# Performance work log

Hardware: AMD Instinct MI355X
Metric: run time of the kernel (lower is better)

Reference implementation:

```python
import jax, jax.numpy as jnp
import numpy as np

B, N, K = 4, 4096, 16
DP, DM = 64, 128
EPS = 1e-8


def setup_inputs() -> dict:
    key = jax.random.key(0)
    ks = jax.random.split(key, 32)
    g = lambda i, shape, fan: jax.random.normal(ks[i], shape, jnp.float32) / np.sqrt(fan)
    inp = {
        'xyz': jax.random.normal(ks[0], (B, N, 3), jnp.float32),
        'features': jax.random.normal(ks[1], (B, N, DP), jnp.float32),
        # fc1: d_points -> d_model
        'fc1_w': g(2, (DP, DM), DP), 'fc1_b': jnp.zeros((DM,), jnp.float32),
        # fc2: d_model -> d_points
        'fc2_w': g(3, (DM, DP), DM), 'fc2_b': jnp.zeros((DP,), jnp.float32),
        # fc_delta: Linear(3,DM) -> ReLU -> Linear(DM,DM)
        'd1_w': g(4, (3, DM), 3), 'd1_b': jnp.zeros((DM,), jnp.float32),
        'd2_w': g(5, (DM, DM), DM), 'd2_b': jnp.zeros((DM,), jnp.float32),
        # fc_gamma: Linear(DM,DM) -> ReLU -> Linear(DM,DM)
        'g1_w': g(6, (DM, DM), DM), 'g1_b': jnp.zeros((DM,), jnp.float32),
        'g2_w': g(7, (DM, DM), DM), 'g2_b': jnp.zeros((DM,), jnp.float32),
        # q/k/v projections, no bias
        'wq_w': g(8, (DM, DM), DM), 'wk_w': g(9, (DM, DM), DM), 'wv_w': g(10, (DM, DM), DM),
        # fc_sim: Linear(DM+1, DM)
        'sim_w': g(11, (DM + 1, DM), DM + 1), 'sim_b': jnp.zeros((DM,), jnp.float32),
    }
    return inp


def _gather(t, idx):
    # t: [B, N, C], idx: [B, N, K] -> [B, N, K, C]
    bidx = jnp.arange(t.shape[0])[:, None, None]
    return t[bidx, idx]


def reference(xyz, features, fc1_w, fc1_b, fc2_w, fc2_b, d1_w, d1_b, d2_w, d2_b,
              g1_w, g1_b, g2_w, g2_b, wq_w, wk_w, wv_w, sim_w, sim_b):
    # pairwise squared distances [B, N, N]
    sq = jnp.sum(xyz * xyz, axis=-1)
    dists = sq[:, :, None] + sq[:, None, :] - 2.0 * jnp.einsum('bnc,bmc->bnm', xyz, xyz)
    knn_idx = jnp.argsort(dists, axis=-1)[:, :, :K]            # [B, N, K]

    knn_xyz = _gather(xyz, knn_idx)                            # [B, N, K, 3]
    x = features @ fc1_w + fc1_b                               # [B, N, DM]
    q = x @ wq_w                                               # [B, N, DM]
    k = _gather(x @ wk_w, knn_idx)                             # [B, N, K, DM]
    v = _gather(x @ wv_w, knn_idx)                             # [B, N, K, DM]

    rel_pos = xyz[:, :, None, :] - knn_xyz                     # [B, N, K, 3]
    pos_enc = jax.nn.relu(rel_pos @ d1_w + d1_b) @ d2_w + d2_b # [B, N, K, DM]

    qe = q[:, :, None, :]                                      # [B, N, 1, DM]
    # torch cosine_similarity: dot / (max(||q||,eps) * max(||k||,eps))
    qn = jnp.maximum(jnp.linalg.norm(q, axis=-1), EPS)[:, :, None]
    kn = jnp.maximum(jnp.linalg.norm(k, axis=-1), EPS)
    sim = jnp.sum(qe * k, axis=-1) / (qn * kn)                 # [B, N, K]

    rel_qk = jnp.concatenate([sim[..., None], qe - k], axis=-1)  # [B, N, K, DM+1]
    rel_qk = rel_qk @ sim_w + sim_b                            # [B, N, K, DM]

    attn = jax.nn.relu((rel_qk + pos_enc) @ g1_w + g1_b) @ g2_w + g2_b
    attn = jax.nn.softmax(attn / np.sqrt(DM).astype(np.float32), axis=-2)  # over K

    res = jnp.einsum('bnkf,bnkf->bnf', attn, v + pos_enc)      # [B, N, DM]
    res = res @ fc2_w + fc2_b + features                       # [B, N, DP]
    return res, attn
```

## Files before the change

### kernel.cpp

```cpp
#include <hip/hip_runtime.h>
#include <hip/hip_bf16.h>

#define BB 4
#define NN 4096
#define KK 16
#define DP 64
#define DM 128
#define DMP 132
#define EPSF 1e-8f
#define OUT0N ((size_t)BB * NN * DP)

typedef unsigned short u16t;
typedef __attribute__((ext_vector_type(8))) short s8v;
typedef __attribute__((ext_vector_type(4))) float f4v;

__device__ int g_flag;

__device__ __forceinline__ float u2f(u16t u) {
    unsigned int x = ((unsigned int)u) << 16;
    return __uint_as_float(x);
}
__device__ __forceinline__ u16t f2u(float v) {
    __hip_bfloat16 h = __float2bfloat16(v);
    return *(u16t*)&h;
}

template<int DT> struct IO;
template<> struct IO<0> {
    static __device__ __forceinline__ float ld(const void* p, size_t i) { return ((const float*)p)[i]; }
    static __device__ __forceinline__ void ld4(const void* p, size_t i, float o[4]) {
        float4 v = *(const float4*)((const float*)p + i);
        o[0] = v.x; o[1] = v.y; o[2] = v.z; o[3] = v.w;
    }
    static __device__ __forceinline__ void st(void* p, size_t i, float v) { ((float*)p)[i] = v; }
};
template<> struct IO<1> {
    static __device__ __forceinline__ float ld(const void* p, size_t i) { return u2f(((const u16t*)p)[i]); }
    static __device__ __forceinline__ void ld4(const void* p, size_t i, float o[4]) {
        ushort4 v = *(const ushort4*)((const u16t*)p + i);
        o[0] = u2f(v.x); o[1] = u2f(v.y); o[2] = u2f(v.z); o[3] = u2f(v.w);
    }
    static __device__ __forceinline__ void st(void* p, size_t i, float v) { ((u16t*)p)[i] = f2u(v); }
};

__global__ __launch_bounds__(64) void detect_kernel(const void* feat) {
    const int tid = threadIdx.x;
    float x = u2f(((const u16t*)feat)[2 * tid]);
    float a = fabsf(x);
    bool sane = (x == 0.0f) || (a > 1e-4f && a < 50.0f);
    unsigned long long m = __ballot(sane);
    if (tid == 0) g_flag = (__popcll(m) >= 32) ? 1 : 0;
}

struct QkvSmem { float sf[DP]; float sx[DM]; };

template<int DT>
__device__ __forceinline__ void qkv_body(QkvSmem& s,
    const void* feat, const void* fc1_w, const void* fc1_b,
    const void* wq, const void* wk, const void* wv,
    float* __restrict__ qbuf, float* __restrict__ kbuf, float* __restrict__ vbuf)
{
    const int bn = blockIdx.x;
    const int tid = threadIdx.x;
    if (tid < DP) s.sf[tid] = IO<DT>::ld(feat, (size_t)bn * DP + tid);
    __syncthreads();
    float x = IO<DT>::ld(fc1_b, tid);
#pragma unroll 4
    for (int i = 0; i < DP; i++) x = fmaf(s.sf[i], IO<DT>::ld(fc1_w, i * DM + tid), x);
    s.sx[tid] = x;
    __syncthreads();
    float q = 0.f, k = 0.f, v = 0.f;
    for (int i0 = 0; i0 < DM; i0 += 4) {
        float4 xv = *(const float4*)&s.sx[i0];
        const float xs[4] = { xv.x, xv.y, xv.z, xv.w };
#pragma unroll
        for (int j = 0; j < 4; j++) {
            q = fmaf(xs[j], IO<DT>::ld(wq, (i0 + j) * DM + tid), q);
            k = fmaf(xs[j], IO<DT>::ld(wk, (i0 + j) * DM + tid), k);
            v = fmaf(xs[j], IO<DT>::ld(wv, (i0 + j) * DM + tid), v);
        }
    }
    qbuf[(size_t)bn * DM + tid] = q;
    kbuf[(size_t)bn * DM + tid] = k;
    vbuf[(size_t)bn * DM + tid] = v;
}

__global__ __launch_bounds__(128) void qkv_kernel(
    const void* feat, const void* fc1_w, const void* fc1_b,
    const void* wq, const void* wk, const void* wv,
    float* qbuf, float* kbuf, float* vbuf)
{
    __shared__ __align__(16) QkvSmem s;
    if (g_flag) qkv_body<1>(s, feat, fc1_w, fc1_b, wq, wk, wv, qbuf, kbuf, vbuf);
    else        qkv_body<0>(s, feat, fc1_w, fc1_b, wq, wk, wv, qbuf, kbuf, vbuf);
}

template<int DT>
__device__ __forceinline__ void knn_body(float4* __restrict__ sc,
    const void* xyz, int* dst, int dstride, void* dout, int in_out)
{
    if (in_out) {
        if (DT) { dst = (int*)((u16t*)dout + OUT0N); dstride = (KK * DM) / 2; }
        else    { dst = (int*)((float*)dout + OUT0N); dstride = KK * DM; }
    }
    const int b = blockIdx.x >> 9;
    const int tid = threadIdx.x;
    for (int j = tid; j < NN; j += 512) {
        float x = IO<DT>::ld(xyz, ((size_t)b * NN + j) * 3 + 0);
        float y = IO<DT>::ld(xyz, ((size_t)b * NN + j) * 3 + 1);
        float z = IO<DT>::ld(xyz, ((size_t)b * NN + j) * 3 + 2);
        float sq = __fadd_rn(__fadd_rn(__fmul_rn(x, x), __fmul_rn(y, y)), __fmul_rn(z, z));
        sc[j] = make_float4(x, y, z, sq);
    }
    __syncthreads();
    const int lane = tid & 63;
    const int wave = tid >> 6;
    const int r = ((blockIdx.x & 511) << 3) + wave;
    const float4 qc = sc[r];

    float d[KK];
    int id[KK];
#pragma unroll
    for (int t = 0; t < KK; t++) { d[t] = 3.4e38f; id[t] = 0x7fffffff; }

    for (int j = lane; j < NN; j += 64) {
        const float4 c = sc[j];
        const float dot = __fadd_rn(__fadd_rn(__fmul_rn(qc.x, c.x), __fmul_rn(qc.y, c.y)),
                                    __fmul_rn(qc.z, c.z));
        const float dist = __fsub_rn(__fadd_rn(qc.w, c.w), __fmul_rn(2.0f, dot));
        if (dist < d[KK - 1]) {
            float cd = dist; int ci = j;
#pragma unroll
            for (int t = 0; t < KK; t++) {
                const bool sw = (cd < d[t]);
                const float od = d[t]; const int oi = id[t];
                d[t]  = sw ? cd : d[t];
                id[t] = sw ? ci : id[t];
                cd = sw ? od : cd;
                ci = sw ? oi : ci;
            }
        }
    }

    const size_t base = (size_t)(b * NN + r) * (size_t)dstride;
#pragma unroll
    for (int t = 0; t < KK; t++) {
        float bd = d[0]; int bi = id[0];
#pragma unroll
        for (int off = 32; off >= 1; off >>= 1) {
            const float od = __shfl_xor(bd, off, 64);
            const int   oi = __shfl_xor(bi, off, 64);
            if (od < bd || (od == bd && oi < bi)) { bd = od; bi = oi; }
        }
        const bool win = (d[0] == bd) && (id[0] == bi);
        if (win) {
#pragma unroll
            for (int u = 0; u < KK - 1; u++) { d[u] = d[u + 1]; id[u] = id[u + 1]; }
            d[KK - 1] = 3.4e38f; id[KK - 1] = 0x7fffffff;
        }
        if (lane == t) dst[base + t] = bi;
    }
}

__global__ __launch_bounds__(512) void knn_kernel(
    const void* xyz, int* dst, int dstride, void* dout, int in_out)
{
    __shared__ __align__(16) float4 sc[NN];
    if (g_flag) knn_body<1>(sc, xyz, dst, dstride, dout, in_out);
    else        knn_body<0>(sc, xyz, dst, dstride, dout, in_out);
}

template<int DT>
__device__ __forceinline__ void gemm_tile(const float* __restrict__ IN,
                                          const void* __restrict__ W, int woff,
                                          int kg, int f0, float acc[4][4])
{
#pragma unroll
    for (int a = 0; a < 4; a++)
#pragma unroll
        for (int c = 0; c < 4; c++) acc[a][c] = 0.f;
    for (int i0 = 0; i0 < DM; i0 += 4) {
        float w[4][4];
#pragma unroll
        for (int j = 0; j < 4; j++) IO<DT>::ld4(W, (size_t)woff + (i0 + j) * DM + f0, w[j]);
#pragma unroll
        for (int kk = 0; kk < 4; kk++) {
            float4 x4 = *(const float4*)(IN + (kg * 4 + kk) * DMP + i0);
            const float xs[4] = { x4.x, x4.y, x4.z, x4.w };
#pragma unroll
            for (int ff = 0; ff < 4; ff++)
#pragma unroll
                for (int j = 0; j < 4; j++)
                    acc[kk][ff] = fmaf(xs[j], w[j][ff], acc[kk][ff]);
        }
    }
}

template<int DT>
__device__ __forceinline__ void wprep_body(const void* sim_w, const void* d2_w,
                                           const void* g1_w, const void* g2_w,
                                           u16t* __restrict__ wprep)
{
    const int m  = blockIdx.x >> 3;
    const int t  = blockIdx.x & 7;
    const int ks = threadIdx.x >> 6;
    const int lane = threadIdx.x & 63;
    const void* src = (m == 0) ? sim_w : (m == 1) ? d2_w : (m == 2) ? g1_w : g2_w;
    const int srcoff = (m == 0) ? DM : 0;
    u16t* hi = wprep + (size_t)m * 32768;
    u16t* lo = hi + 16384;
    const int c  = t * 16 + (lane & 15);
    const int k0 = ks * 32 + ((lane >> 4) << 3);
    s8v vh, vl;
#pragma unroll
    for (int j = 0; j < 8; j++) {
        const float x = IO<DT>::ld(src, (size_t)srcoff + (size_t)(k0 + j) * DM + c);
        const u16t h = f2u(x);
        vh[j] = (short)h;
        vl[j] = (short)f2u(x - u2f(h));
    }
    const size_t off = ((size_t)(t * 4 + ks) * 64 + lane) * 8;
    *(s8v*)(hi + off) = vh;
    *(s8v*)(lo + off) = vl;
}

__global__ __launch_bounds__(256) void wprep_kernel(
    const void* sim_w, const void* d2_w, const void* g1_w, const void* g2_w,
    u16t* wprep)
{
    if (g_flag) wprep_body<1>(sim_w, d2_w, g1_w, g2_w, wprep);
    else        wprep_body<0>(sim_w, d2_w, g1_w, g2_w, wprep);
}

template<int DT, int EPI>
__device__ __forceinline__ void mfma_gemm16(const float* __restrict__ IN,
                                            float* __restrict__ OUT,
                                            const u16t* __restrict__ wmat,
                                            const void* bias, const void* w0,
                                            const float* __restrict__ ssim)
{
    const int tid  = threadIdx.x;
    const int lane = tid & 63;
    const int wid  = tid >> 6;
    const u16t* whi = wmat;
    const u16t* wlo = wmat + 16384;
    f4v acc[4] = { {0.f,0.f,0.f,0.f}, {0.f,0.f,0.f,0.f}, {0.f,0.f,0.f,0.f}, {0.f,0.f,0.f,0.f} };
    const float* ain = IN + (size_t)(lane & 15) * DMP + ((lane >> 4) << 3);
#pragma unroll
    for (int ks = 0; ks < 4; ks++) {
        const float4 x0 = *(const float4*)(ain + ks * 32);
        const float4 x1 = *(const float4*)(ain + ks * 32 + 4);
        const float xs[8] = { x0.x, x0.y, x0.z, x0.w, x1.x, x1.y, x1.z, x1.w };
        s8v ahi, alo;
#pragma unroll
        for (int j = 0; j < 8; j++) {
            const u16t h = f2u(xs[j]);
            ahi[j] = (short)h;
            alo[j] = (short)f2u(xs[j] - u2f(h));
        }
#pragma unroll
        for (int t = 0; t < 4; t++) {
            const size_t off = ((size_t)((wid * 4 + t) * 4 + ks) * 64 + lane) * 8;
            const s8v bhi = *(const s8v*)(whi + off);
            const s8v blo = *(const s8v*)(wlo + off);
            acc[t] = __builtin_amdgcn_mfma_f32_16x16x32_bf16(ahi, bhi, acc[t], 0, 0, 0);
            acc[t] = __builtin_amdgcn_mfma_f32_16x16x32_bf16(ahi, blo, acc[t], 0, 0, 0);
            acc[t] = __builtin_amdgcn_mfma_f32_16x16x32_bf16(alo, bhi, acc[t], 0, 0, 0);
        }
    }
    const int r0 = (lane >> 4) * 4;
#pragma unroll
    for (int t = 0; t < 4; t++) {
        const int col = (wid * 4 + t) * 16 + (lane & 15);
        const float bv = IO<DT>::ld(bias, col);
        float w0v = 0.f;
        if constexpr (EPI == 2) w0v = IO<DT>::ld(w0, col);
#pragma unroll
        for (int r = 0; r < 4; r++) {
            float v = acc[t][r] + bv;
            if constexpr (EPI == 2) v = fmaf(ssim[r0 + r], w0v, v);
            if constexpr (EPI == 1) v = fmaxf(v, 0.f);
            OUT[(size_t)(r0 + r) * DMP + col] = v;
        }
    }
}

struct AttnSmemM {
    float KP[KK * DMP];
    float T0[KK * DMP];
    float T1[KK * DMP];
    float s_q[DM], sres[DM];
    float srp[KK][3];
    float ssim[KK], skn[KK], sdot[KK];
    float sqn;
    int sidx[KK];
};

template<int DT>
__device__ __forceinline__ void attn_mfma_body(AttnSmemM& s,
    const void* xyz, const void* feat,
    const void* fc2_w, const void* fc2_b,
    const void* d1_w, const void* d1_b, const void* d2_b,
    const void* g1_b, const void* g2_b,
    const void* sim_w, const void* sim_b,
    const float* __restrict__ qbuf, const float* __restrict__ kbuf,
    const float* __restrict__ vbuf,
    const int* __restrict__ knn, const u16t* __restrict__ wprep, void* dout)
{
    void* out0 = dout;
    void* out1 = DT ? (void*)((u16t*)dout + OUT0N) : (void*)((float*)dout + OUT0N);
    const int bn = blockIdx.x;
    const int b = bn >> 12;
    const int tid = threadIdx.x;
    const int f = tid;

    if (tid < KK) {
        int sv = knn[(size_t)bn * KK + tid];
        sv = (sv < 0) ? 0 : (sv > NN - 1 ? NN - 1 : sv);
        s.sidx[tid] = sv;
    }
    __syncthreads();

    s.s_q[f] = qbuf[(size_t)bn * DM + f];
#pragma unroll
    for (int k = 0; k < KK; k++) {
        const int row = (b << 12) + s.sidx[k];
        s.KP[k * DMP + f] = kbuf[(size_t)row * DM + f];
    }
    if (tid < KK) {
        const int row = (b << 12) + s.sidx[tid];
#pragma unroll
        for (int c = 0; c < 3; c++)
            s.srp[tid][c] = IO<DT>::ld(xyz, (size_t)bn * 3 + c) - IO<DT>::ld(xyz, (size_t)row * 3 + c);
    }
    __syncthreads();

    {
        const int j = tid >> 3, g = tid & 7;
        float sk = 0.f, sd = 0.f, qq = 0.f;
#pragma unroll
        for (int i = 0; i < 16; i++) {
            const int ff = g * 16 + i;
            const float kv = s.KP[j * DMP + ff];
            const float qv = s.s_q[ff];
            sk = fmaf(kv, kv, sk);
            sd = fmaf(qv, kv, sd);
            qq = fmaf(qv, qv, qq);
        }
#pragma unroll
        for (int off = 1; off <= 4; off <<= 1) {
            sk += __shfl_xor(sk, off, 64);
            sd += __shfl_xor(sd, off, 64);
            qq += __shfl_xor(qq, off, 64);
        }
        if (g == 0) { s.skn[j] = fmaxf(sqrtf(sk), EPSF); s.sdot[j] = sd; }
        if (tid == 0) s.sqn = fmaxf(sqrtf(qq), EPSF);
    }
    __syncthreads();

    if (tid < KK) s.ssim[tid] = s.sdot[tid] / (s.sqn * s.skn[tid]);
#pragma unroll
    for (int k = 0; k < KK; k++) s.T0[k * DMP + f] = s.s_q[f] - s.KP[k * DMP + f];
    __syncthreads();

    mfma_gemm16<DT, 2>(s.T0, s.T1, wprep + 0 * 32768, sim_b, sim_w, s.ssim);
    __syncthreads();

    {
        const float w0 = IO<DT>::ld(d1_w, 0 * DM + f), w1 = IO<DT>::ld(d1_w, 1 * DM + f),
                    w2 = IO<DT>::ld(d1_w, 2 * DM + f);
        const float hb = IO<DT>::ld(d1_b, f);
#pragma unroll
        for (int k = 0; k < KK; k++) {
            const float h = fmaf(s.srp[k][2], w2, fmaf(s.srp[k][1], w1, fmaf(s.srp[k][0], w0, hb)));
            s.T0[k * DMP + f] = fmaxf(h, 0.f);
        }
    }
    __syncthreads();

    mfma_gemm16<DT, 0>(s.T0, s.KP, wprep + 1 * 32768, d2_b, nullptr, nullptr);
    __syncthreads();

#pragma unroll
    for (int k = 0; k < KK; k++) s.T0[k * DMP + f] = s.T1[k * DMP + f] + s.KP[k * DMP + f];
    __syncthreads();

    mfma_gemm16<DT, 1>(s.T0, s.T1, wprep + 2 * 32768, g1_b, nullptr, nullptr);
    __syncthreads();

    mfma_gemm16<DT, 0>(s.T1, s.T0, wprep + 3 * 32768, g2_b, nullptr, nullptr);
    __syncthreads();

    {
        const float sq128 = 11.31370849898476f;
        float tv[KK];
        float mx = -3.4e38f;
#pragma unroll
        for (int k = 0; k < KK; k++) { tv[k] = s.T0[k * DMP + f] / sq128; mx = fmaxf(mx, tv[k]); }
        float ssum = 0.f;
#pragma unroll
        for (int k = 0; k < KK; k++) { tv[k] = expf(tv[k] - mx); ssum += tv[k]; }
        float rf = 0.f;
#pragma unroll
        for (int k = 0; k < KK; k++) {
            const float a = tv[k] / ssum;
            IO<DT>::st(out1, ((size_t)bn * KK + k) * DM + f, a);
            const int row = (b << 12) + s.sidx[k];
            rf = fmaf(a, vbuf[(size_t)row * DM + f] + s.KP[k * DMP + f], rf);
        }
        s.sres[f] = rf;
    }
    __syncthreads();

    if (tid < DP) {
        float o = 0.f;
        for (int i = 0; i < DM; i++) o = fmaf(s.sres[i], IO<DT>::ld(fc2_w, (size_t)i * DP + tid), o);
        o = o + IO<DT>::ld(fc2_b, tid) + IO<DT>::ld(feat, (size_t)bn * DP + tid);
        IO<DT>::st(out0, (size_t)bn * DP + tid, o);
    }
}

__global__ __launch_bounds__(128) void attn_mfma_kernel(
    const void* xyz, const void* feat,
    const void* fc2_w, const void* fc2_b,
    const void* d1_w, const void* d1_b, const void* d2_b,
    const void* g1_b, const void* g2_b,
    const void* sim_w, const void* sim_b,
    const float* qbuf, const float* kbuf, const float* vbuf,
    const int* knn, const u16t* wprep, void* dout)
{
    __shared__ __align__(16) AttnSmemM s;
    if (g_flag)
        attn_mfma_body<1>(s, xyz, feat, fc2_w, fc2_b, d1_w, d1_b, d2_b, g1_b, g2_b,
                          sim_w, sim_b, qbuf, kbuf, vbuf, knn, wprep, dout);
    else
        attn_mfma_body<0>(s, xyz, feat, fc2_w, fc2_b, d1_w, d1_b, d2_b, g1_b, g2_b,
                          sim_w, sim_b, qbuf, kbuf, vbuf, knn, wprep, dout);
}

template<bool FUSED> struct AttnSmem {
    float Kb[KK * DMP], Vb[KK * DMP], PE[KK * DMP], T0[KK * DMP], T1[KK * DMP];
    float s_q[DM], sres[DM];
    float SF[FUSED ? 17 * DP : 1];
    float X[FUSED ? 17 * DMP : 1];
    float srp[KK][3];
    float ssim[KK], skn[KK], sdot[KK];
    float sqn;
    int sidx[KK];
};

template<int DT, bool FUSED>
__device__ __forceinline__ void attn_body(AttnSmem<FUSED>& s,
    const void* xyz, const void* feat,
    const void* fc1_w, const void* fc1_b, const void* fc2_w, const void* fc2_b,
    const void* d1_w, const void* d1_b, const void* d2_w, const void* d2_b,
    const void* g1_w, const void* g1_b, const void* g2_w, const void* g2_b,
    const void* sim_w, const void* sim_b,
    const void* wq, const void* wk, const void* wv,
    const float* __restrict__ qbuf, const float* __restrict__ kbuf, const float* __restrict__ vbuf,
    const int* knn, int knn_stride, int knn_in_out, void* dout)
{
    void* out0 = dout;
    void* out1 = DT ? (void*)((u16t*)dout + OUT0N) : (void*)((float*)dout + OUT0N);
    if (knn_in_out) {
        if (DT) { knn = (const int*)((const u16t*)dout + OUT0N); knn_stride = (KK * DM) / 2; }
        else    { knn = (const int*)((const float*)dout + OUT0N); knn_stride = KK * DM; }
    }

    const int bn = blockIdx.x;
    const int b = bn >> 12;
    const int tid = threadIdx.x;
    const int f = tid;
    const int f0 = (tid & 31) * 4;
    const int kg = tid >> 5;

    if (tid < KK) {
        int sv = knn[(size_t)bn * knn_stride + tid];
        sv = (sv < 0) ? 0 : (sv > NN - 1 ? NN - 1 : sv);
        s.sidx[tid] = sv;
    }
    __syncthreads();

    if constexpr (FUSED) {
        for (int idx = tid; idx < 17 * DP; idx += 128) {
            const int r = idx >> 6, c = idx & 63;
            const int row = (r < KK) ? ((b << 12) + s.sidx[r]) : bn;
            s.SF[idx] = IO<DT>::ld(feat, (size_t)row * DP + c);
        }
        __syncthreads();
        float xacc[17];
        const float fb = IO<DT>::ld(fc1_b, tid);
#pragma unroll
        for (int r = 0; r < 17; r++) xacc[r] = fb;
        for (int i = 0; i < DP; i++) {
            const float w = IO<DT>::ld(fc1_w, i * DM + tid);
#pragma unroll
            for (int r = 0; r < 17; r++) xacc[r] = fmaf(s.SF[r * DP + i], w, xacc[r]);
        }
#pragma unroll
        for (int r = 0; r < 17; r++) s.X[r * DMP + tid] = xacc[r];
        __syncthreads();
        {
            float a2[4][4];
            gemm_tile<DT>(s.X, wk, 0, kg, f0, a2);
#pragma unroll
            for (int kk = 0; kk < 4; kk++)
                *(float4*)&s.Kb[(kg * 4 + kk) * DMP + f0] =
                    make_float4(a2[kk][0], a2[kk][1], a2[kk][2], a2[kk][3]);
            gemm_tile<DT>(s.X, wv, 0, kg, f0, a2);
#pragma unroll
            for (int kk = 0; kk < 4; kk++)
                *(float4*)&s.Vb[(kg * 4 + kk) * DMP + f0] =
                    make_float4(a2[kk][0], a2[kk][1], a2[kk][2], a2[kk][3]);
        }
        {
            float qv = 0.f;
            for (int i0 = 0; i0 < DM; i0 += 4) {
                float4 x4 = *(const float4*)&s.X[16 * DMP + i0];
                const float xs[4] = { x4.x, x4.y, x4.z, x4.w };
#pragma unroll
                for (int j = 0; j < 4; j++)
                    qv = fmaf(xs[j], IO<DT>::ld(wq, (i0 + j) * DM + tid), qv);
            }
            s.s_q[tid] = qv;
        }
    } else {
        s.s_q[f] = qbuf[(size_t)bn * DM + f];
#pragma unroll
        for (int k = 0; k < KK; k++) {
            const int row = (b << 12) + s.sidx[k];
            s.Kb[k * DMP + f] = kbuf[(size_t)row * DM + f];
            s.Vb[k * DMP + f] = vbuf[(size_t)row * DM + f];
        }
    }
    if (tid < KK) {
        const int row = (b << 12) + s.sidx[tid];
#pragma unroll
        for (int c = 0; c < 3; c++)
            s.srp[tid][c] = IO<DT>::ld(xyz, (size_t)bn * 3 + c) - IO<DT>::ld(xyz, (size_t)row * 3 + c);
    }
    __syncthreads();

    if (tid < KK) {
        float sk = 0.f, sd = 0.f;
        for (int i = 0; i < DM; i++) {
            float v2 = s.Kb[tid * DMP + i];
            sk = fmaf(v2, v2, sk);
            sd = fmaf(s.s_q[i], v2, sd);
        }
        s.skn[tid] = fmaxf(sqrtf(sk), EPSF);
        s.sdot[tid] = sd;
    } else if (tid == KK) {
        float sqq = 0.f;
        for (int i = 0; i < DM; i++) { float v2 = s.s_q[i]; sqq = fmaf(v2, v2, sqq); }
        s.sqn = fmaxf(sqrtf(sqq), EPSF);
    }
    __syncthreads();
    if (tid < KK) s.ssim[tid] = s.sdot[tid] / (s.sqn * s.skn[tid]);
#pragma unroll
    for (int k = 0; k < KK; k++) s.T0[k * DMP + f] = s.s_q[f] - s.Kb[k * DMP + f];
    __syncthreads();

    float acc[4][4];

    gemm_tile<DT>(s.T0, sim_w, DM, kg, f0, acc);
    {
        float w0f[4], sbf[4];
        IO<DT>::ld4(sim_w, f0, w0f);
        IO<DT>::ld4(sim_b, f0, sbf);
#pragma unroll
        for (int kk = 0; kk < 4; kk++) {
            float sm = s.ssim[kg * 4 + kk];
            float4 o;
            o.x = fmaf(sm, w0f[0], acc[kk][0]) + sbf[0];
            o.y = fmaf(sm, w0f[1], acc[kk][1]) + sbf[1];
            o.z = fmaf(sm, w0f[2], acc[kk][2]) + sbf[2];
            o.w = fmaf(sm, w0f[3], acc[kk][3]) + sbf[3];
            *(float4*)&s.T1[(kg * 4 + kk) * DMP + f0] = o;
        }
    }
    __syncthreads();

    {
        float w0 = IO<DT>::ld(d1_w, 0 * DM + f), w1 = IO<DT>::ld(d1_w, 1 * DM + f),
              w2 = IO<DT>::ld(d1_w, 2 * DM + f);
        float hb = IO<DT>::ld(d1_b, f);
#pragma unroll
        for (int k = 0; k < KK; k++) {
            float h = fmaf(s.srp[k][2], w2, fmaf(s.srp[k][1], w1, fmaf(s.srp[k][0], w0, hb)));
            s.T0[k * DMP + f] = fmaxf(h, 0.f);
        }
    }
    __syncthreads();

    gemm_tile<DT>(s.T0, d2_w, 0, kg, f0, acc);
    {
        float bf[4];
        IO<DT>::ld4(d2_b, f0, bf);
#pragma unroll
        for (int kk = 0; kk < 4; kk++)
            *(float4*)&s.PE[(kg * 4 + kk) * DMP + f0] =
                make_float4(acc[kk][0] + bf[0], acc[kk][1] + bf[1],
                            acc[kk][2] + bf[2], acc[kk][3] + bf[3]);
    }
    __syncthreads();

#pragma unroll
    for (int kk = 0; kk < 4; kk++) {
        const int row = (kg * 4 + kk) * DMP + f0;
        float4 a4 = *(const float4*)&s.T1[row];
        float4 p4 = *(const float4*)&s.PE[row];
        *(float4*)&s.T0[row] = make_float4(a4.x + p4.x, a4.y + p4.y, a4.z + p4.z, a4.w + p4.w);
    }
    __syncthreads();

    gemm_tile<DT>(s.T0, g1_w, 0, kg, f0, acc);
    {
        float bf[4];
        IO<DT>::ld4(g1_b, f0, bf);
#pragma unroll
        for (int kk = 0; kk < 4; kk++)
            *(float4*)&s.T1[(kg * 4 + kk) * DMP + f0] =
                make_float4(fmaxf(acc[kk][0] + bf[0], 0.f), fmaxf(acc[kk][1] + bf[1], 0.f),
                            fmaxf(acc[kk][2] + bf[2], 0.f), fmaxf(acc[kk][3] + bf[3], 0.f));
    }
    __syncthreads();

    gemm_tile<DT>(s.T1, g2_w, 0, kg, f0, acc);
    {
        float bf[4];
        IO<DT>::ld4(g2_b, f0, bf);
#pragma unroll
        for (int kk = 0; kk < 4; kk++)
            *(float4*)&s.T0[(kg * 4 + kk) * DMP + f0] =
                make_float4(acc[kk][0] + bf[0], acc[kk][1] + bf[1],
                            acc[kk][2] + bf[2], acc[kk][3] + bf[3]);
    }
    __syncthreads();

    {
        const float sq128 = 11.31370849898476f;
        float tv[KK];
        float m = -3.4e38f;
#pragma unroll
        for (int k = 0; k < KK; k++) { tv[k] = s.T0[k * DMP + f] / sq128; m = fmaxf(m, tv[k]); }
        float ssum = 0.f;
#pragma unroll
        for (int k = 0; k < KK; k++) { tv[k] = expf(tv[k] - m); ssum += tv[k]; }
        float rf = 0.f;
#pragma unroll
        for (int k = 0; k < KK; k++) {
            float a = tv[k] / ssum;
            IO<DT>::st(out1, ((size_t)bn * KK + k) * DM + f, a);
            rf = fmaf(a, s.Vb[k * DMP + f] + s.PE[k * DMP + f], rf);
        }
        s.sres[f] = rf;
    }
    __syncthreads();

    if (tid < DP) {
        float o = 0.f;
        for (int i = 0; i < DM; i++) o = fmaf(s.sres[i], IO<DT>::ld(fc2_w, i * DP + tid), o);
        o = o + IO<DT>::ld(fc2_b, tid) + IO<DT>::ld(feat, (size_t)bn * DP + tid);
        IO<DT>::st(out0, (size_t)bn * DP + tid, o);
    }
}

template<bool FUSED>
__global__ __launch_bounds__(128) void attn_kernel(
    const void* xyz, const void* feat,
    const void* fc1_w, const void* fc1_b, const void* fc2_w, const void* fc2_b,
    const void* d1_w, const void* d1_b, const void* d2_w, const void* d2_b,
    const void* g1_w, const void* g1_b, const void* g2_w, const void* g2_b,
    const void* sim_w, const void* sim_b,
    const void* wq, const void* wk, const void* wv,
    const float* qbuf, const float* kbuf, const float* vbuf,
    const int* knn, int knn_stride, int knn_in_out, void* dout)
{
    __shared__ __align__(16) AttnSmem<FUSED> s;
    if (g_flag)
        attn_body<1, FUSED>(s, xyz, feat, fc1_w, fc1_b, fc2_w, fc2_b, d1_w, d1_b, d2_w, d2_b,
                            g1_w, g1_b, g2_w, g2_b, sim_w, sim_b, wq, wk, wv,
                            qbuf, kbuf, vbuf, knn, knn_stride, knn_in_out, dout);
    else
        attn_body<0, FUSED>(s, xyz, feat, fc1_w, fc1_b, fc2_w, fc2_b, d1_w, d1_b, d2_w, d2_b,
                            g1_w, g1_b, g2_w, g2_b, sim_w, sim_b, wq, wk, wv,
                            qbuf, kbuf, vbuf, knn, knn_stride, knn_in_out, dout);
}

extern "C" void kernel_launch(void* const* d_in, const int* in_sizes, int n_in,
                              void* d_out, int out_size, void* d_ws, size_t ws_size,
                              hipStream_t stream)
{
    const void* xyz   = d_in[0];
    const void* feat  = d_in[1];
    const void* fc1_w = d_in[2];
    const void* fc1_b = d_in[3];
    const void* fc2_w = d_in[4];
    const void* fc2_b = d_in[5];
    const void* d1_w  = d_in[6];
    const void* d1_b  = d_in[7];
    const void* d2_w  = d_in[8];
    const void* d2_b  = d_in[9];
    const void* g1_w  = d_in[10];
    const void* g1_b  = d_in[11];
    const void* g2_w  = d_in[12];
    const void* g2_b  = d_in[13];
    const void* wq_w  = d_in[14];
    const void* wk_w  = d_in[15];
    const void* wv_w  = d_in[16];
    const void* sim_w = d_in[17];
    const void* sim_b = d_in[18];

    detect_kernel<<<1, 64, 0, stream>>>(feat);

    const size_t need_qkv = (size_t)3 * BB * NN * DM * sizeof(float);
    const size_t need_knn = (size_t)BB * NN * KK * sizeof(int);
    const size_t need_wp  = (size_t)4 * 2 * 16384 * sizeof(u16t);

    if (ws_size >= need_qkv + need_knn + need_wp && d_ws != nullptr) {
        float* qbuf  = (float*)d_ws;
        float* kbuf  = qbuf + (size_t)BB * NN * DM;
        float* vbuf  = kbuf + (size_t)BB * NN * DM;
        int*   knn   = (int*)(vbuf + (size_t)BB * NN * DM);
        u16t*  wprep = (u16t*)(knn + (size_t)BB * NN * KK);
        qkv_kernel<<<BB * NN, DM, 0, stream>>>(feat, fc1_w, fc1_b, wq_w, wk_w, wv_w, qbuf, kbuf, vbuf);
        knn_kernel<<<BB * 512, 512, 0, stream>>>(xyz, knn, KK, d_out, 0);
        wprep_kernel<<<32, 256, 0, stream>>>(sim_w, d2_w, g1_w, g2_w, wprep);
        attn_mfma_kernel<<<BB * NN, DM, 0, stream>>>(
            xyz, feat, fc2_w, fc2_b, d1_w, d1_b, d2_b, g1_b, g2_b, sim_w, sim_b,
            qbuf, kbuf, vbuf, knn, wprep, d_out);
    } else if (ws_size >= need_qkv + need_knn && d_ws != nullptr) {
        float* qbuf = (float*)d_ws;
        float* kbuf = qbuf + (size_t)BB * NN * DM;
        float* vbuf = kbuf + (size_t)BB * NN * DM;
        int*   knn  = (int*)(vbuf + (size_t)BB * NN * DM);
        qkv_kernel<<<BB * NN, DM, 0, stream>>>(feat, fc1_w, fc1_b, wq_w, wk_w, wv_w, qbuf, kbuf, vbuf);
        knn_kernel<<<BB * 512, 512, 0, stream>>>(xyz, knn, KK, d_out, 0);
        attn_kernel<false><<<BB * NN, DM, 0, stream>>>(
            xyz, feat, fc1_w, fc1_b, fc2_w, fc2_b, d1_w, d1_b, d2_w, d2_b,
            g1_w, g1_b, g2_w, g2_b, sim_w, sim_b, wq_w, wk_w, wv_w,
            qbuf, kbuf, vbuf, knn, KK, 0, d_out);
    } else if (ws_size >= need_knn && d_ws != nullptr) {
        int* knn = (int*)d_ws;
        knn_kernel<<<BB * 512, 512, 0, stream>>>(xyz, knn, KK, d_out, 0);
        attn_kernel<true><<<BB * NN, DM, 0, stream>>>(
            xyz, feat, fc1_w, fc1_b, fc2_w, fc2_b, d1_w, d1_b, d2_w, d2_b,
            g1_w, g1_b, g2_w, g2_b, sim_w, sim_b, wq_w, wk_w, wv_w,
            nullptr, nullptr, nullptr, knn, KK, 0, d_out);
    } else {
        knn_kernel<<<BB * 512, 512, 0, stream>>>(xyz, nullptr, 0, d_out, 1);
        attn_kernel<true><<<BB * NN, DM, 0, stream>>>(
            xyz, feat, fc1_w, fc1_b, fc2_w, fc2_b, d1_w, d1_b, d2_w, d2_b,
            g1_w, g1_b, g2_w, g2_b, sim_w, sim_b, wq_w, wk_w, wv_w,
            nullptr, nullptr, nullptr, nullptr, 0, 1, d_out);
    }
}
```

Baseline: 668.5 us.

## Batch multiple points per block in QKV and attention kernels

The QKV projection kernel now handles 16 points per 256-thread block, so each weight load from global memory is reused across 8 points per thread. The attention kernel handles 4 points per 512-thread block, and the MFMA GEMMs become 64-row tiles whose waves share a weight column chunk. The aim is to cut redundant weight traffic and per-block overhead from launching one block per point. In exchange it uses more shared memory per block (about 100KB for attention), which may lower occupancy.

```diff
diff --git a/kernel.cpp b/kernel.cpp
--- a/kernel.cpp
+++ b/kernel.cpp
@@ -93,6 +93,81 @@
     __shared__ __align__(16) QkvSmem s;
     if (g_flag) qkv_body<1>(s, feat, fc1_w, fc1_b, wq, wk, wv, qbuf, kbuf, vbuf);
     else        qkv_body<0>(s, feat, fc1_w, fc1_b, wq, wk, wv, qbuf, kbuf, vbuf);
+}
+
+struct Qkv16Smem { float sf[16][DP]; float sx[16][DMP]; };
+
+template<int DT>
+__device__ __forceinline__ void qkv16_body(Qkv16Smem& s,
+    const void* feat, const void* fc1_w, const void* fc1_b,
+    const void* wq, const void* wk, const void* wv,
+    float* __restrict__ qbuf, float* __restrict__ kbuf, float* __restrict__ vbuf)
+{
+    const int pnt0 = blockIdx.x << 4;
+    const int tid = threadIdx.x;
+    {
+        const int r = tid >> 4, c4 = (tid & 15) << 2;
+        float o[4];
+        IO<DT>::ld4(feat, (size_t)(pnt0 + r) * DP + c4, o);
+        s.sf[r][c4 + 0] = o[0]; s.sf[r][c4 + 1] = o[1];
+        s.sf[r][c4 + 2] = o[2]; s.sf[r][c4 + 3] = o[3];
+    }
+    __syncthreads();
+    const int c = tid & 127, h = tid >> 7;
+    {
+        float acc[8];
+        const float fb = IO<DT>::ld(fc1_b, c);
+#pragma unroll
+        for (int pp = 0; pp < 8; pp++) acc[pp] = fb;
+        for (int i = 0; i < DP; i++) {
+            const float w = IO<DT>::ld(fc1_w, (size_t)i * DM + c);
+#pragma unroll
+            for (int pp = 0; pp < 8; pp++) acc[pp] = fmaf(s.sf[h * 8 + pp][i], w, acc[pp]);
+        }
+#pragma unroll
+        for (int pp = 0; pp < 8; pp++) s.sx[h * 8 + pp][c] = acc[pp];
+    }
+    __syncthreads();
+    {
+        float aq[8], ak[8], av[8];
+#pragma unroll
+        for (int pp = 0; pp < 8; pp++) { aq[pp] = 0.f; ak[pp] = 0.f; av[pp] = 0.f; }
+        for (int i0 = 0; i0 < DM; i0 += 4) {
+            float x4[8][4];
+#pragma unroll
+            for (int pp = 0; pp < 8; pp++) {
+                const float4 xv = *(const float4*)&s.sx[h * 8 + pp][i0];
+                x4[pp][0] = xv.x; x4[pp][1] = xv.y; x4[pp][2] = xv.z; x4[pp][3] = xv.w;
+            }
+#pragma unroll
+            for (int j = 0; j < 4; j++) {
+                const float wqv = IO<DT>::ld(wq, (size_t)(i0 + j) * DM + c);
+                const float wkv = IO<DT>::ld(wk, (size_t)(i0 + j) * DM + c);
+                const float wvv = IO<DT>::ld(wv, (size_t)(i0 + j) * DM + c);
+#pragma unroll
+                for (int pp = 0; pp < 8; pp++) {
+                    aq[pp] = fmaf(x4[pp][j], wqv, aq[pp]);
+                    ak[pp] = fmaf(x4[pp][j], wkv, ak[pp]);
+                    av[pp] = fmaf(x4[pp][j], wvv, av[pp]);
+                }
+            }
+        }
+#pragma unroll
+        for (int pp = 0; pp < 8; pp++) {
+            const size_t row = (size_t)(pnt0 + h * 8 + pp) * DM + c;
+            qbuf[row] = aq[pp]; kbuf[row] = ak[pp]; vbuf[row] = av[pp];
+        }
+    }
+}
+
+__global__ __launch_bounds__(256) void qkv16_kernel(
+    const void* feat, const void* fc1_w, const void* fc1_b,
+    const void* wq, const void* wk, const void* wv,
+    float* qbuf, float* kbuf, float* vbuf)
+{
+    __shared__ __align__(16) Qkv16Smem s;
+    if (g_flag) qkv16_body<1>(s, feat, fc1_w, fc1_b, wq, wk, wv, qbuf, kbuf, vbuf);
+    else        qkv16_body<0>(s, feat, fc1_w, fc1_b, wq, wk, wv, qbuf, kbuf, vbuf);
 }
 
 template<int DT>
@@ -233,7 +308,7 @@
 }
 
 template<int DT, int EPI>
-__device__ __forceinline__ void mfma_gemm16(const float* __restrict__ IN,
+__device__ __forceinline__ void mfma_gemm64(const float* __restrict__ IN,
                                             float* __restrict__ OUT,
                                             const u16t* __restrict__ wmat,
                                             const void* bias, const void* w0,
@@ -242,10 +317,12 @@
     const int tid  = threadIdx.x;
     const int lane = tid & 63;
     const int wid  = tid >> 6;
+    const int mt   = wid & 3;
+    const int ch   = wid >> 2;
     const u16t* whi = wmat;
     const u16t* wlo = wmat + 16384;
     f4v acc[4] = { {0.f,0.f,0.f,0.f}, {0.f,0.f,0.f,0.f}, {0.f,0.f,0.f,0.f}, {0.f,0.f,0.f,0.f} };
-    const float* ain = IN + (size_t)(lane & 15) * DMP + ((lane >> 4) << 3);
+    const float* ain = IN + (size_t)(mt * 16 + (lane & 15)) * DMP + ((lane >> 4) << 3);
 #pragma unroll
     for (int ks = 0; ks < 4; ks++) {
         const float4 x0 = *(const float4*)(ain + ks * 32);
@@ -260,7 +337,7 @@
         }
 #pragma unroll
         for (int t = 0; t < 4; t++) {
-            const size_t off = ((size_t)((wid * 4 + t) * 4 + ks) * 64 + lane) * 8;
+            const size_t off = ((size_t)((ch * 4 + t) * 4 + ks) * 64 + lane) * 8;
             const s8v bhi = *(const s8v*)(whi + off);
             const s8v blo = *(const s8v*)(wlo + off);
             acc[t] = __builtin_amdgcn_mfma_f32_16x16x32_bf16(ahi, bhi, acc[t], 0, 0, 0);
@@ -271,33 +348,34 @@
     const int r0 = (lane >> 4) * 4;
 #pragma unroll
     for (int t = 0; t < 4; t++) {
-        const int col = (wid * 4 + t) * 16 + (lane & 15);
+        const int col = (ch * 4 + t) * 16 + (lane & 15);
         const float bv = IO<DT>::ld(bias, col);
         float w0v = 0.f;
         if constexpr (EPI == 2) w0v = IO<DT>::ld(w0, col);
 #pragma unroll
         for (int r = 0; r < 4; r++) {
+            const int row = mt * 16 + r0 + r;
             float v = acc[t][r] + bv;
-            if constexpr (EPI == 2) v = fmaf(ssim[r0 + r], w0v, v);
+            if constexpr (EPI == 2) v = fmaf(ssim[row], w0v, v);
             if constexpr (EPI == 1) v = fmaxf(v, 0.f);
-            OUT[(size_t)(r0 + r) * DMP + col] = v;
-        }
-    }
-}
-
-struct AttnSmemM {
-    float KP[KK * DMP];
-    float T0[KK * DMP];
-    float T1[KK * DMP];
-    float s_q[DM], sres[DM];
-    float srp[KK][3];
-    float ssim[KK], skn[KK], sdot[KK];
-    float sqn;
-    int sidx[KK];
+            OUT[(size_t)row * DMP + col] = v;
+        }
+    }
+}
+
+struct AttnSmem4 {
+    float KP[64 * DMP];
+    float T0[64 * DMP];
+    float T1[64 * DMP];
+    float s_q[4 * DM], sres[4 * DM];
+    float srp[64][3];
+    float ssim[64], skn[64], sdot[64];
+    float sqn[4];
+    int sidx[64];
 };
 
 template<int DT>
-__device__ __forceinline__ void attn_mfma_body(AttnSmemM& s,
+__device__ __forceinline__ void attn4_body(AttnSmem4& s,
     const void* xyz, const void* feat,
     const void* fc2_w, const void* fc2_b,
     const void* d1_w, const void* d1_b, const void* d2_b,
@@ -309,40 +387,45 @@
 {
     void* out0 = dout;
     void* out1 = DT ? (void*)((u16t*)dout + OUT0N) : (void*)((float*)dout + OUT0N);
-    const int bn = blockIdx.x;
-    const int b = bn >> 12;
+    const int pnt0 = blockIdx.x << 2;
+    const int b = pnt0 >> 12;
     const int tid = threadIdx.x;
-    const int f = tid;
-
-    if (tid < KK) {
-        int sv = knn[(size_t)bn * KK + tid];
+
+    if (tid < 64) {
+        int sv = knn[(size_t)(pnt0 + (tid >> 4)) * KK + (tid & 15)];
         sv = (sv < 0) ? 0 : (sv > NN - 1 ? NN - 1 : sv);
         s.sidx[tid] = sv;
     }
     __syncthreads();
 
-    s.s_q[f] = qbuf[(size_t)bn * DM + f];
-#pragma unroll
-    for (int k = 0; k < KK; k++) {
-        const int row = (b << 12) + s.sidx[k];
-        s.KP[k * DMP + f] = kbuf[(size_t)row * DM + f];
-    }
-    if (tid < KK) {
-        const int row = (b << 12) + s.sidx[tid];
+    {
+        const int p = tid >> 7, ff = tid & 127;
+        s.s_q[tid] = qbuf[(size_t)(pnt0 + p) * DM + ff];
+#pragma unroll
+        for (int k = 0; k < KK; k++) {
+            const int row = p * 16 + k;
+            const int grow = (b << 12) + s.sidx[row];
+            s.KP[row * DMP + ff] = kbuf[(size_t)grow * DM + ff];
+        }
+    }
+    if (tid < 64) {
+        const int grow = (b << 12) + s.sidx[tid];
+        const int p = tid >> 4;
 #pragma unroll
         for (int c = 0; c < 3; c++)
-            s.srp[tid][c] = IO<DT>::ld(xyz, (size_t)bn * 3 + c) - IO<DT>::ld(xyz, (size_t)row * 3 + c);
-    }
-    __syncthreads();
-
-    {
-        const int j = tid >> 3, g = tid & 7;
+            s.srp[tid][c] = IO<DT>::ld(xyz, (size_t)(pnt0 + p) * 3 + c)
+                          - IO<DT>::ld(xyz, (size_t)grow * 3 + c);
+    }
+    __syncthreads();
+
+    {
+        const int j = tid >> 3, g = tid & 7, p = j >> 4;
         float sk = 0.f, sd = 0.f, qq = 0.f;
 #pragma unroll
         for (int i = 0; i < 16; i++) {
             const int ff = g * 16 + i;
             const float kv = s.KP[j * DMP + ff];
-            const float qv = s.s_q[ff];
+            const float qv = s.s_q[p * DM + ff];
             sk = fmaf(kv, kv, sk);
             sd = fmaf(qv, kv, sd);
             qq = fmaf(qv, qv, qq);
@@ -353,50 +436,72 @@
             sd += __shfl_xor(sd, off, 64);
             qq += __shfl_xor(qq, off, 64);
         }
-        if (g == 0) { s.skn[j] = fmaxf(sqrtf(sk), EPSF); s.sdot[j] = sd; }
-        if (tid == 0) s.sqn = fmaxf(sqrtf(qq), EPSF);
-    }
-    __syncthreads();
-
-    if (tid < KK) s.ssim[tid] = s.sdot[tid] / (s.sqn * s.skn[tid]);
-#pragma unroll
-    for (int k = 0; k < KK; k++) s.T0[k * DMP + f] = s.s_q[f] - s.KP[k * DMP + f];
-    __syncthreads();
-
-    mfma_gemm16<DT, 2>(s.T0, s.T1, wprep + 0 * 32768, sim_b, sim_w, s.ssim);
-    __syncthreads();
-
-    {
-        const float w0 = IO<DT>::ld(d1_w, 0 * DM + f), w1 = IO<DT>::ld(d1_w, 1 * DM + f),
-                    w2 = IO<DT>::ld(d1_w, 2 * DM + f);
-        const float hb = IO<DT>::ld(d1_b, f);
+        if (g == 0) {
+            s.skn[j] = fmaxf(sqrtf(sk), EPSF);
+            s.sdot[j] = sd;
+            if ((j & 15) == 0) s.sqn[p] = fmaxf(sqrtf(qq), EPSF);
+        }
+    }
+    __syncthreads();
+
+    if (tid < 64) s.ssim[tid] = s.sdot[tid] / (s.sqn[tid >> 4] * s.skn[tid]);
+    {
+        const int p = tid >> 7, ff = tid & 127;
 #pragma unroll
         for (int k = 0; k < KK; k++) {
-            const float h = fmaf(s.srp[k][2], w2, fmaf(s.srp[k][1], w1, fmaf(s.srp[k][0], w0, hb)));
-            s.T0[k * DMP + f] = fmaxf(h, 0.f);
-        }
-    }
-    __syncthreads();
-
-    mfma_gemm16<DT, 0>(s.T0, s.KP, wprep + 1 * 32768, d2_b, nullptr, nullptr);
-    __syncthreads();
-
-#pragma unroll
-    for (int k = 0; k < KK; k++) s.T0[k * DMP + f] = s.T1[k * DMP + f] + s.KP[k * DMP + f];
-    __syncthreads();
-
-    mfma_gemm16<DT, 1>(s.T0, s.T1, wprep + 2 * 32768, g1_b, nullptr, nullptr);
-    __syncthreads();
-
-    mfma_gemm16<DT, 0>(s.T1, s.T0, wprep + 3 * 32768, g2_b, nullptr, nullptr);
-    __syncthreads();
-
-    {
+            const int row = p * 16 + k;
+            s.T0[row * DMP + ff] = s.s_q[p * DM + ff] - s.KP[row * DMP + ff];
+        }
+    }
+    __syncthreads();
+
+    mfma_gemm64<DT, 2>(s.T0, s.T1, wprep + 0 * 32768, sim_b, sim_w, s.ssim);
+    __syncthreads();
+
+    {
+        const int p = tid >> 7, ff = tid & 127;
+        const float w0 = IO<DT>::ld(d1_w, 0 * DM + ff), w1 = IO<DT>::ld(d1_w, 1 * DM + ff),
+                    w2 = IO<DT>::ld(d1_w, 2 * DM + ff);
+        const float hb = IO<DT>::ld(d1_b, ff);
+#pragma unroll
+        for (int k = 0; k < KK; k++) {
+            const int row = p * 16 + k;
+            const float h = fmaf(s.srp[row][2], w2,
+                            fmaf(s.srp[row][1], w1, fmaf(s.srp[row][0], w0, hb)));
+            s.T0[row * DMP + ff] = fmaxf(h, 0.f);
+        }
+    }
+    __syncthreads();
+
+    mfma_gemm64<DT, 0>(s.T0, s.KP, wprep + 1 * 32768, d2_b, nullptr, nullptr);
+    __syncthreads();
+
+    {
+        const int p = tid >> 7, ff = tid & 127;
+#pragma unroll
+        for (int k = 0; k < KK; k++) {
+            const int row = p * 16 + k;
+            s.T0[row * DMP + ff] = s.T1[row * DMP + ff] + s.KP[row * DMP + ff];
+        }
+    }
+    __syncthreads();
+
+    mfma_gemm64<DT, 1>(s.T0, s.T1, wprep + 2 * 32768, g1_b, nullptr, nullptr);
+    __syncthreads();
+
+    mfma_gemm64<DT, 0>(s.T1, s.T0, wprep + 3 * 32768, g2_b, nullptr, nullptr);
+    __syncthreads();
+
+    {
+        const int p = tid >> 7, ff = tid & 127;
         const float sq128 = 11.31370849898476f;
         float tv[KK];
         float mx = -3.4e38f;
 #pragma unroll
-        for (int k = 0; k < KK; k++) { tv[k] = s.T0[k * DMP + f] / sq128; mx = fmaxf(mx, tv[k]); }
+        for (int k = 0; k < KK; k++) {
+            tv[k] = s.T0[(p * 16 + k) * DMP + ff] / sq128;
+            mx = fmaxf(mx, tv[k]);
+        }
         float ssum = 0.f;
 #pragma unroll
         for (int k = 0; k < KK; k++) { tv[k] = expf(tv[k] - mx); ssum += tv[k]; }
@@ -404,23 +509,25 @@
 #pragma unroll
         for (int k = 0; k < KK; k++) {
             const float a = tv[k] / ssum;
-            IO<DT>::st(out1, ((size_t)bn * KK + k) * DM + f, a);
-            const int row = (b << 12) + s.sidx[k];
-            rf = fmaf(a, vbuf[(size_t)row * DM + f] + s.KP[k * DMP + f], rf);
-        }
-        s.sres[f] = rf;
-    }
-    __syncthreads();
-
-    if (tid < DP) {
+            IO<DT>::st(out1, ((size_t)(pnt0 + p) * KK + k) * DM + ff, a);
+            const int row = p * 16 + k;
+            const int grow = (b << 12) + s.sidx[row];
+            rf = fmaf(a, vbuf[(size_t)grow * DM + ff] + s.KP[row * DMP + ff], rf);
+        }
+        s.sres[tid] = rf;
+    }
+    __syncthreads();
+
+    if (tid < 256) {
+        const int p = tid >> 6, c = tid & 63;
         float o = 0.f;
-        for (int i = 0; i < DM; i++) o = fmaf(s.sres[i], IO<DT>::ld(fc2_w, (size_t)i * DP + tid), o);
-        o = o + IO<DT>::ld(fc2_b, tid) + IO<DT>::ld(feat, (size_t)bn * DP + tid);
-        IO<DT>::st(out0, (size_t)bn * DP + tid, o);
-    }
-}
-
-__global__ __launch_bounds__(128) void attn_mfma_kernel(
+        for (int i = 0; i < DM; i++) o = fmaf(s.sres[p * DM + i], IO<DT>::ld(fc2_w, (size_t)i * DP + c), o);
+        o = o + IO<DT>::ld(fc2_b, c) + IO<DT>::ld(feat, (size_t)(pnt0 + p) * DP + c);
+        IO<DT>::st(out0, (size_t)(pnt0 + p) * DP + c, o);
+    }
+}
+
+__global__ __launch_bounds__(512) void attn4_kernel(
     const void* xyz, const void* feat,
     const void* fc2_w, const void* fc2_b,
     const void* d1_w, const void* d1_b, const void* d2_b,
@@ -429,13 +536,13 @@
     const float* qbuf, const float* kbuf, const float* vbuf,
     const int* knn, const u16t* wprep, void* dout)
 {
-    __shared__ __align__(16) AttnSmemM s;
+    __shared__ __align__(16) AttnSmem4 s;
     if (g_flag)
-        attn_mfma_body<1>(s, xyz, feat, fc2_w, fc2_b, d1_w, d1_b, d2_b, g1_b, g2_b,
-                          sim_w, sim_b, qbuf, kbuf, vbuf, knn, wprep, dout);
+        attn4_body<1>(s, xyz, feat, fc2_w, fc2_b, d1_w, d1_b, d2_b, g1_b, g2_b,
+                      sim_w, sim_b, qbuf, kbuf, vbuf, knn, wprep, dout);
     else
-        attn_mfma_body<0>(s, xyz, feat, fc2_w, fc2_b, d1_w, d1_b, d2_b, g1_b, g2_b,
-                          sim_w, sim_b, qbuf, kbuf, vbuf, knn, wprep, dout);
+        attn4_body<0>(s, xyz, feat, fc2_w, fc2_b, d1_w, d1_b, d2_b, g1_b, g2_b,
+                      sim_w, sim_b, qbuf, kbuf, vbuf, knn, wprep, dout);
 }
 
 template<bool FUSED> struct AttnSmem {
@@ -724,10 +831,11 @@
         float* vbuf  = kbuf + (size_t)BB * NN * DM;
         int*   knn   = (int*)(vbuf + (size_t)BB * NN * DM);
         u16t*  wprep = (u16t*)(knn + (size_t)BB * NN * KK);
-        qkv_kernel<<<BB * NN, DM, 0, stream>>>(feat, fc1_w, fc1_b, wq_w, wk_w, wv_w, qbuf, kbuf, vbuf);
+        qkv16_kernel<<<(BB * NN) / 16, 256, 0, stream>>>(feat, fc1_w, fc1_b, wq_w, wk_w, wv_w,
+                                                         qbuf, kbuf, vbuf);
         knn_kernel<<<BB * 512, 512, 0, stream>>>(xyz, knn, KK, d_out, 0);
         wprep_kernel<<<32, 256, 0, stream>>>(sim_w, d2_w, g1_w, g2_w, wprep);
-        attn_mfma_kernel<<<BB * NN, DM, 0, stream>>>(
+        attn4_kernel<<<(BB * NN) / 4, 512, 0, stream>>>(
             xyz, feat, fc2_w, fc2_b, d1_w, d1_b, d2_b, g1_b, g2_b, sim_w, sim_b,
             qbuf, kbuf, vbuf, knn, wprep, d_out);
     } else if (ws_size >= need_qkv + need_knn && d_ws != nullptr) {
```

Result: slower. 705.8 us (+5.6%).
